# Performance work log

Measured on AMD Instinct MI355X. Metric: run time of the kernel, lower is better.

## Reference

```python
import jax, jax.numpy as jnp
import numpy as np

N = 197          # tokens (== token_count)
B = 64           # batch
D = 768          # d_model
NH = 12          # n_head
GH = 2           # global_heads
HR = NH // GH    # head_ratio = 6
DH = 64          # d_head
QK = GH * DH     # qk_dim = 128
ML = 3           # mask_levels
EPS = 1e-5


def setup_inputs() -> dict:
    key = jax.random.key(0)
    ks = jax.random.split(key, 9)
    s = 1.0 / np.sqrt(D)
    return {
        "h": jax.random.normal(ks[0], (N, B, D), dtype=jnp.float32),
        "masks": jax.random.uniform(ks[1], (N, N, ML), dtype=jnp.float32),
        "Wq": jax.random.normal(ks[2], (QK, D), dtype=jnp.float32) * s,
        "Wk": jax.random.normal(ks[3], (QK, D), dtype=jnp.float32) * s,
        "Wv": jax.random.normal(ks[4], (NH * DH, D), dtype=jnp.float32) * s,
        "Wo": jax.random.normal(ks[5], (D, NH * DH), dtype=jnp.float32) * s,
        "mask_proj": jnp.ones((ML, NH), dtype=jnp.float32),
        "ln_gamma": jnp.ones((D,), dtype=jnp.float32),
        "ln_beta": jnp.zeros((D,), dtype=jnp.float32),
    }


def reference(h, masks, Wq, Wk, Wv, Wo, mask_proj, ln_gamma, ln_beta):
    scale = 1.0 / np.sqrt(DH)
    # projections (seq-first layout [N, B, ...])
    q = (h @ Wq.T).reshape(N, B, GH, DH)
    k = (h @ Wk.T).reshape(N, B, GH, DH)
    v = (h @ Wv.T).reshape(N, B, NH, DH)
    # global-head scores: [B, GH, i, j]
    score = jnp.einsum('ibgd,jbgd->bgij', q, k) * scale
    # learned mask mix: [i, j, NH] -> [GH, i, j, HR] (g-major head split, matches torch reshape)
    mw = jnp.einsum('ijl,ln->ijn', masks, mask_proj)
    mw = mw.reshape(N, N, GH, HR).transpose(2, 0, 1, 3)
    # broadcast each global head to HR local heads: [B, GH, i, j, HR]
    attn = score[..., None] * mw[None]
    attn = attn.transpose(0, 1, 4, 2, 3).reshape(B, NH, N, N)  # head = g*HR + r
    prob = jax.nn.softmax(attn, axis=-1)
    # AV: [i, B, NH, DH] -> [N, B, NH*DH]
    vec = jnp.einsum('bnij,jbnd->ibnd', prob, v).reshape(N, B, NH * DH)
    out = vec @ Wo.T
    # post-LN residual
    x = h + out
    mu = jnp.mean(x, axis=-1, keepdims=True)
    var = jnp.var(x, axis=-1, keepdims=True)
    return ln_gamma * (x - mu) / jnp.sqrt(var + EPS) + ln_beta
```

## Files before the change

### kernel.cpp

```cpp
#include <hip/hip_runtime.h>
#include <hip/hip_bf16.h>
#include <stdint.h>

#define NTOK 197
#define NPAD 224
#define BATCH 64
#define DMODEL 768
#define NHEAD 12
#define GHEAD 2
#define HRATIO 6
#define DHEAD 64
#define QKDIM 128
#define LNEPS 1e-5f
#define MROWS (NTOK * BATCH)
#define MPAD 12672
#define NKC 24
#define NBAND 99

using f32x4 = __attribute__((ext_vector_type(4))) float;
using s16x8 = __attribute__((ext_vector_type(8))) short;
using s16x4 = __attribute__((ext_vector_type(4))) short;

__device__ __forceinline__ short f2bf(float f) {
  unsigned int x = __float_as_uint(f);
  return (short)((x + 0x7fffu + ((x >> 16) & 1u)) >> 16);
}

__device__ __forceinline__ float bf2f(short s) {
  return __uint_as_float((unsigned)(unsigned short)s << 16);
}

__device__ __forceinline__ void gld16(void* lds, const void* g) {
  __builtin_amdgcn_global_load_lds(
      (const __attribute__((address_space(1))) unsigned int*)g,
      (__attribute__((address_space(3))) unsigned int*)lds, 16, 0, 0);
}

#define NBH (NBAND * NKC)
#define NBQ (8 * NKC)
#define NBW (6 * NKC)
__global__ __launch_bounds__(256)
void prep_kernel(const float* __restrict__ h, const float* __restrict__ Wq,
                 const float* __restrict__ Wk, const float* __restrict__ Wv,
                 const float* __restrict__ Wo, short* __restrict__ hf,
                 short* __restrict__ Wqkvf, short* __restrict__ Wof) {
  const int bb = blockIdx.x, t = threadIdx.x;
  int band, kc, which;
  if (bb < NBH) { which = 0; band = bb / NKC; kc = bb - band * NKC; }
  else if (bb < NBH + NBQ) { int i = bb - NBH; which = 1; band = i / NKC; kc = i - band * NKC; }
  else { int i = bb - NBH - NBQ; which = 2; band = i / NKC; kc = i - band * NKC; }
  short* dstS = (which == 0 ? hf : which == 1 ? Wqkvf : Wof) +
                ((size_t)(band * NKC + kc) * 8) * 512;
#pragma unroll
  for (int uu = 0; uu < 2; ++uu) {
    int u = t + uu * 256;
    int frag = u >> 6, l = u & 63;
    int rl = frag * 16 + (l & 15);
    int k0 = kc * 32 + ((l >> 4) & 3) * 8;
    float4 a = {0, 0, 0, 0}, c = {0, 0, 0, 0};
    if (which == 0) {
      int row = band * 128 + rl;
      if (row < MROWS) {
        const float* p = h + (size_t)row * DMODEL + k0;
        a = *(const float4*)p; c = *(const float4*)(p + 4);
      }
    } else if (which == 1) {
      int row = band * 128 + rl;
      const float* src = (row < 128) ? Wq + (size_t)row * DMODEL
                       : (row < 256) ? Wk + (size_t)(row - 128) * DMODEL
                                     : Wv + (size_t)(row - 256) * DMODEL;
      a = *(const float4*)(src + k0); c = *(const float4*)(src + k0 + 4);
    } else {
      const float* p = Wo + (size_t)(band * 128 + rl) * DMODEL + k0;
      a = *(const float4*)p; c = *(const float4*)(p + 4);
    }
    s16x8 o;
    o[0] = f2bf(a.x); o[1] = f2bf(a.y); o[2] = f2bf(a.z); o[3] = f2bf(a.w);
    o[4] = f2bf(c.x); o[5] = f2bf(c.y); o[6] = f2bf(c.z); o[7] = f2bf(c.w);
    *(s16x8*)(dstS + (size_t)u * 8) = o;
  }
}

template<int AM>
__global__ __launch_bounds__(256, 3)
void gemm_bstage_kernel(const short* __restrict__ Af, const short* __restrict__ Bf,
                        short* __restrict__ Cout, int M, int NC) {
  __shared__ short Bs[12 * 4 * 512];
  const int tid = threadIdx.x;
  const int nwg = gridDim.x * gridDim.y;
  const int orig = blockIdx.y * gridDim.x + blockIdx.x;
  const int qq = nwg >> 3, rr = nwg & 7;
  const int xcd = orig & 7, sidx = orig >> 3;
  const int wg = (xcd < rr ? xcd * (qq + 1) : rr * (qq + 1) + (xcd - rr) * qq) + sidx;
  const int cb = wg % gridDim.x;
  const int rb = wg / gridDim.x;

  const int w = tid >> 6, l = tid & 63;
  const int lm = l & 15, lh = l >> 4;

  const short* Bg = Bf + (size_t)(cb >> 1) * NKC * 4096 +
                    ((cb & 1) * 4 + w) * 512 + l * 8;
  const short* paF = Af + (size_t)rb * NKC * 4096 + (2 * w) * 512 + l * 8;
  const short* paR = Af + (size_t)(rb * 128 + w * 32 + lm) * DMODEL + lh * 8;

  f32x4 acc[2][4] = {};

#pragma unroll
  for (int half = 0; half < 2; ++half) {
    if (half) __syncthreads();
#pragma unroll
    for (int p = 0; p < 12; ++p)
      gld16(Bs + (p * 4 + w) * 512 + l * 8, Bg + (size_t)(half * 12 + p) * 4096);
    __syncthreads();
#pragma unroll
    for (int kcl = 0; kcl < 12; ++kcl) {
      const int kc = half * 12 + kcl;
      s16x8 af[2], bf[4];
      if (AM == 0) {
#pragma unroll
        for (int m = 0; m < 2; ++m)
          af[m] = *(const s16x8*)(paF + (size_t)kc * 4096 + m * 512);
      } else {
#pragma unroll
        for (int m = 0; m < 2; ++m)
          af[m] = *(const s16x8*)(paR + (size_t)m * 16 * DMODEL + kc * 32);
      }
#pragma unroll
      for (int n = 0; n < 4; ++n)
        bf[n] = *(const s16x8*)(Bs + (kcl * 4 + n) * 512 + l * 8);
#pragma unroll
      for (int m = 0; m < 2; ++m)
#pragma unroll
        for (int n = 0; n < 4; ++n)
          acc[m][n] = __builtin_amdgcn_mfma_f32_16x16x32_bf16(af[m], bf[n],
                                                              acc[m][n], 0, 0, 0);
    }
  }

#pragma unroll
  for (int m = 0; m < 2; ++m) {
#pragma unroll
    for (int r = 0; r < 4; ++r) {
      int row = rb * 128 + w * 32 + m * 16 + lh * 4 + r;
      if (row < M) {
#pragma unroll
        for (int n = 0; n < 4; ++n) {
          int col = cb * 64 + n * 16 + lm;
          Cout[(size_t)row * NC + col] = f2bf(acc[m][n][r]);
        }
      }
    }
  }
}

__global__ __launch_bounds__(256)
void packall_kernel(const short* __restrict__ Cb, const float* __restrict__ masks,
                    const float* __restrict__ mproj, short* __restrict__ qp,
                    short* __restrict__ kp, short* __restrict__ vT,
                    float* __restrict__ mwp) {
  __shared__ short Vs[NPAD][DHEAD + 1];
  const int bb = blockIdx.x, t = threadIdx.x;
  if (bb < 256) {
    int b = bb >> 2, g = (bb >> 1) & 1, which = bb & 1;
    short* dst = (which ? kp : qp) + ((size_t)b * GHEAD + g) * NPAD * 64;
    int d = t & 63, iofs = t >> 6;
    for (int i0 = 0; i0 < NPAD; i0 += 4) {
      int i = i0 + iofs;
      short v = 0;
      if (i < NTOK)
        v = Cb[(size_t)(i * BATCH + b) * 1024 + which * QKDIM + g * DHEAD + d];
      int dd = which ? ((((d >> 3) ^ (i & 7)) << 3) | (d & 7)) : d;
      dst[i * 64 + dd] = v;
    }
  } else if (bb < 1024) {
    int vv = bb - 256;
    int b = vv / 12, n = vv - b * 12;
    int d = t & 63, iofs = t >> 6;
    for (int i0 = 0; i0 < NPAD; i0 += 4) {
      int i = i0 + iofs;
      short v = 0;
      if (i < NTOK)
        v = Cb[(size_t)(i * BATCH + b) * 1024 + 256 + n * DHEAD + d];
      Vs[i][d] = v;
    }
    __syncthreads();
    short* dst = vT + ((size_t)b * NHEAD + n) * DHEAD * NPAD;
    int sub = t & 63, dr = t >> 6;
    for (int d0 = 0; d0 < DHEAD; d0 += 4) {
      if (sub < 56) {
        int dd = d0 + dr, j0 = sub * 4;
        s16x4 o;
        o[0] = Vs[j0][dd]; o[1] = Vs[j0 + 1][dd];
        o[2] = Vs[j0 + 2][dd]; o[3] = Vs[j0 + 3][dd];
        *(s16x4*)(dst + dd * NPAD + j0) = o;
      }
    }
  } else {
    int e = (bb - 1024) * 256 + t;
    int n = e >> 12;
    int rem = e & 4095;
    int i = rem >> 4, lm = rem & 15;
    float p0 = mproj[n], p1 = mproj[NHEAD + n], p2 = mproj[2 * NHEAD + n];
    float vals[16];
#pragma unroll
    for (int jf = 0; jf < 16; ++jf) vals[jf] = 0.f;
    if (i < NTOK) {
#pragma unroll
      for (int jf = 0; jf < 14; ++jf) {
        int col = jf * 16 + lm;
        if (col < NTOK) {
          const float* mp = masks + ((size_t)i * NTOK + col) * 3;
          vals[jf] = 0.125f * (mp[0] * p0 + mp[1] * p1 + mp[2] * p2);
        }
      }
    }
    float* dst = mwp + (size_t)e * 16;
#pragma unroll
    for (int q = 0; q < 4; ++q) {
      float4 o = make_float4(vals[q * 4], vals[q * 4 + 1], vals[q * 4 + 2], vals[q * 4 + 3]);
      *(float4*)(dst + q * 4) = o;
    }
  }
}

__global__ __launch_bounds__(256, 2)
void attn_fused_kernel(const short* __restrict__ qp, const short* __restrict__ kp,
                       const short* __restrict__ vT, const float* __restrict__ mwp,
                       short* __restrict__ vec_b) {
  const int it = blockIdx.x, b = blockIdx.y, g = blockIdx.z;
  __shared__ short Ks[NPAD * 64];
  __shared__ short Pt[64 * 256];
  __shared__ float rsb[64];
  const int t = threadIdx.x, w = t >> 6, l = t & 63;
  const int lm = l & 15, lh = l >> 4, l7 = l & 7;

  const short* qg = qp + ((size_t)b * GHEAD + g) * NPAD * 64;
  const short* kg = kp + ((size_t)b * GHEAD + g) * NPAD * 64;

#pragma unroll
  for (int s = 0; s < 7; ++s)
    gld16(Ks + s * 2048 + t * 8, kg + s * 2048 + t * 8);
  int qrow = it * 64 + w * 16 + lm;
  if (qrow > NPAD - 1) qrow = NPAD - 1;
  s16x8 a0 = *(const s16x8*)(qg + qrow * 64 + lh * 8);
  s16x8 a1 = *(const s16x8*)(qg + qrow * 64 + 32 + lh * 8);
  __syncthreads();

  f32x4 acc[14] = {};
#pragma unroll
  for (int jf = 0; jf < 14; ++jf) {
    s16x8 kf0 = *(const s16x8*)((const char*)Ks + (jf * 16 + lm) * 128 + ((lh ^ l7) << 4));
    s16x8 kf1 = *(const s16x8*)((const char*)Ks + (jf * 16 + lm) * 128 + (((4 + lh) ^ l7) << 4));
    acc[jf] = __builtin_amdgcn_mfma_f32_16x16x32_bf16(a0, kf0, acc[jf], 0, 0, 0);
    acc[jf] = __builtin_amdgcn_mfma_f32_16x16x32_bf16(a1, kf1, acc[jf], 0, 0, 0);
  }

  for (int hh = 0; hh < HRATIO; ++hh) {
    const int n = g * HRATIO + hh;
    const short* vg = vT + ((size_t)b * NHEAD + n) * 64 * NPAD;
    s16x8 vf[7];
#pragma unroll
    for (int ks = 0; ks < 7; ++ks)
      vf[ks] = *(const s16x8*)(vg + (w * 16 + lm) * NPAD + ks * 32 + lh * 8);

#pragma unroll
    for (int r = 0; r < 4; ++r) {
      const int row = w * 16 + lh * 4 + r;
      const int i = it * 64 + row;
      const float* mr = mwp + (((size_t)n * 256 + i) * 16 + lm) * 16;
      f32x4 mv0 = *(const f32x4*)(mr);
      f32x4 mv1 = *(const f32x4*)(mr + 4);
      f32x4 mv2 = *(const f32x4*)(mr + 8);
      f32x4 mv3 = *(const f32x4*)(mr + 12);
      float sum = 0.f;
#pragma unroll
      for (int jf = 0; jf < 13; ++jf) {
        float mwv = (jf < 4) ? mv0[jf] : (jf < 8) ? mv1[jf - 4]
                  : (jf < 12) ? mv2[jf - 8] : mv3[jf - 12];
        float pe = __expf(acc[jf][r] * mwv);
        if (jf == 12 && lm >= 5) pe = 0.f;
        sum += pe;
        int byteoff = row * 512 + (((2 * jf + (lm >> 3)) ^ (row & 7)) << 4) + (lm & 7) * 2;
        *(short*)((char*)Pt + byteoff) = f2bf(pe);
      }
      {
        int byteoff = row * 512 + (((26 + (lm >> 3)) ^ (row & 7)) << 4) + (lm & 7) * 2;
        *(short*)((char*)Pt + byteoff) = 0;
      }
#pragma unroll
      for (int off = 8; off; off >>= 1) sum += __shfl_xor(sum, off);
      if (lm == 0) rsb[row] = 1.f / sum;
    }
    __syncthreads();

    __builtin_amdgcn_s_setprio(1);
    f32x4 oacc[4] = {};
#pragma unroll
    for (int fi = 0; fi < 4; ++fi)
#pragma unroll
      for (int ks = 0; ks < 7; ++ks) {
        s16x8 pa = *(const s16x8*)((const char*)Pt + (fi * 16 + lm) * 512 +
                                   (((ks * 4 + lh) ^ l7) << 4));
        oacc[fi] = __builtin_amdgcn_mfma_f32_16x16x32_bf16(pa, vf[ks], oacc[fi], 0, 0, 0);
      }
    __builtin_amdgcn_s_setprio(0);
#pragma unroll
    for (int fi = 0; fi < 4; ++fi)
#pragma unroll
      for (int r = 0; r < 4; ++r) {
        int ia = it * 64 + fi * 16 + lh * 4 + r;
        if (ia < NTOK) {
          float rsv = rsb[fi * 16 + lh * 4 + r];
          vec_b[((size_t)ia * BATCH + b) * DMODEL + n * 64 + w * 16 + lm] =
              f2bf(oacc[fi][r] * rsv);
        }
      }
    __syncthreads();
  }
}

__global__ __launch_bounds__(256)
void ln_kernel(const float* __restrict__ h, const short* __restrict__ proj_b,
               float* __restrict__ out, const float* __restrict__ gamma,
               const float* __restrict__ beta) {
  const int m = blockIdx.x;
  const float* hrow = h + (size_t)m * DMODEL;
  const short* prow = proj_b + (size_t)m * DMODEL;
  float* orow = out + (size_t)m * DMODEL;
  const int tid = threadIdx.x;
  float v0 = hrow[tid] + bf2f(prow[tid]);
  float v1 = hrow[tid + 256] + bf2f(prow[tid + 256]);
  float v2 = hrow[tid + 512] + bf2f(prow[tid + 512]);
  float s = v0 + v1 + v2;
  float sq = v0 * v0 + v1 * v1 + v2 * v2;
#pragma unroll
  for (int off = 32; off; off >>= 1) {
    s += __shfl_xor(s, off);
    sq += __shfl_xor(sq, off);
  }
  __shared__ float ss[4], ssq[4];
  const int w = tid >> 6, lane = tid & 63;
  if (lane == 0) { ss[w] = s; ssq[w] = sq; }
  __syncthreads();
  s = ss[0] + ss[1] + ss[2] + ss[3];
  sq = ssq[0] + ssq[1] + ssq[2] + ssq[3];
  const float inv = 1.0f / (float)DMODEL;
  float mu = s * inv;
  float var = sq * inv - mu * mu;
  float rstd = rsqrtf(var + LNEPS);
  orow[tid] = gamma[tid] * (v0 - mu) * rstd + beta[tid];
  orow[tid + 256] = gamma[tid + 256] * (v1 - mu) * rstd + beta[tid + 256];
  orow[tid + 512] = gamma[tid + 512] * (v2 - mu) * rstd + beta[tid + 512];
}

extern "C" void kernel_launch(void* const* d_in, const int* in_sizes, int n_in,
                              void* d_out, int out_size, void* d_ws, size_t ws_size,
                              hipStream_t stream) {
  const float* h     = (const float*)d_in[0];
  const float* masks = (const float*)d_in[1];
  const float* Wq    = (const float*)d_in[2];
  const float* Wk    = (const float*)d_in[3];
  const float* Wv    = (const float*)d_in[4];
  const float* Wo    = (const float*)d_in[5];
  const float* mproj = (const float*)d_in[6];
  const float* gamma = (const float*)d_in[7];
  const float* beta  = (const float*)d_in[8];
  float* out = (float*)d_out;

  char* ws = (char*)d_ws;
  size_t o = 0;
  auto alloc = [&](size_t bytes) { size_t r = o; o += (bytes + 255) & ~(size_t)255; return r; };
  short* hf    = (short*)(ws + alloc((size_t)MPAD * DMODEL * 2));
  short* Cb    = (short*)(ws + alloc((size_t)MPAD * 1024 * 2));
  short* Wqkvf = (short*)(ws + alloc((size_t)1024 * DMODEL * 2));
  short* Wof   = (short*)(ws + alloc((size_t)DMODEL * DMODEL * 2));
  short* qp    = (short*)(ws + alloc((size_t)BATCH * GHEAD * NPAD * DHEAD * 2));
  short* kp    = (short*)(ws + alloc((size_t)BATCH * GHEAD * NPAD * DHEAD * 2));
  short* vT    = (short*)(ws + alloc((size_t)BATCH * NHEAD * DHEAD * NPAD * 2));
  float* mwp   = (float*)(ws + alloc((size_t)NHEAD * 256 * 16 * 16 * 4));
  short* vec_b = hf;
  short* proj_b = Cb;

  prep_kernel<<<NBH + NBQ + NBW, 256, 0, stream>>>(h, Wq, Wk, Wv, Wo, hf, Wqkvf, Wof);
  gemm_bstage_kernel<0><<<dim3(1024 / 64, NBAND), 256, 0, stream>>>(
      hf, Wqkvf, Cb, MROWS, 1024);
  packall_kernel<<<1216, 256, 0, stream>>>(Cb, masks, mproj, qp, kp, vT, mwp);
  attn_fused_kernel<<<dim3(4, BATCH, GHEAD), 256, 0, stream>>>(qp, kp, vT, mwp, vec_b);
  gemm_bstage_kernel<1><<<dim3(DMODEL / 64, NBAND), 256, 0, stream>>>(
      vec_b, Wof, proj_b, MROWS, DMODEL);
  ln_kernel<<<MROWS, 256, 0, stream>>>(h, proj_b, out, gamma, beta);
}
```

Baseline: 152.2 us.

## Replace GEMMs with 256x256-tile double-buffered LDS pipeline using 512 threads

The two projection GEMMs now use 256x256 output tiles with 8 waves per block. A and B k-tiles of width 64 are staged into double-buffered LDS through direct global-to-LDS loads, and the next tile is prefetched while MFMAs run on the current one. The prep kernel is reorganised to emit fragments in the matching 256-row, 64-k tile layout, and setprio is raised around the MFMA bursts. Larger tiles give more reuse per byte loaded. The cost is far fewer blocks (200 and 150), which may underfill the GPU's CUs, plus high register pressure from the 8x4 accumulators.

```diff
diff --git a/kernel.cpp b/kernel.cpp
--- a/kernel.cpp
+++ b/kernel.cpp
@@ -13,9 +13,9 @@
 #define QKDIM 128
 #define LNEPS 1e-5f
 #define MROWS (NTOK * BATCH)
-#define MPAD 12672
-#define NKC 24
-#define NBAND 99
+#define MPAD2 12800
+#define NBAND2 50
+#define NKT 12
 
 using f32x4 = __attribute__((ext_vector_type(4))) float;
 using s16x8 = __attribute__((ext_vector_type(8))) short;
@@ -36,56 +36,56 @@
       (__attribute__((address_space(3))) unsigned int*)lds, 16, 0, 0);
 }
 
-#define NBH (NBAND * NKC)
-#define NBQ (8 * NKC)
-#define NBW (6 * NKC)
+#define NT_A (NBAND2 * NKT)
+#define NT_Q (4 * NKT)
+#define NT_W (3 * NKT)
 __global__ __launch_bounds__(256)
 void prep_kernel(const float* __restrict__ h, const float* __restrict__ Wq,
                  const float* __restrict__ Wk, const float* __restrict__ Wv,
                  const float* __restrict__ Wo, short* __restrict__ hf,
                  short* __restrict__ Wqkvf, short* __restrict__ Wof) {
   const int bb = blockIdx.x, t = threadIdx.x;
-  int band, kc, which;
-  if (bb < NBH) { which = 0; band = bb / NKC; kc = bb - band * NKC; }
-  else if (bb < NBH + NBQ) { int i = bb - NBH; which = 1; band = i / NKC; kc = i - band * NKC; }
-  else { int i = bb - NBH - NBQ; which = 2; band = i / NKC; kc = i - band * NKC; }
-  short* dstS = (which == 0 ? hf : which == 1 ? Wqkvf : Wof) +
-                ((size_t)(band * NKC + kc) * 8) * 512;
-#pragma unroll
-  for (int uu = 0; uu < 2; ++uu) {
-    int u = t + uu * 256;
+  int band, kt, which;
+  if (bb < NT_A) { which = 0; band = bb / NKT; kt = bb - band * NKT; }
+  else if (bb < NT_A + NT_Q) { int i = bb - NT_A; which = 1; band = i / NKT; kt = i - band * NKT; }
+  else { int i = bb - NT_A - NT_Q; which = 2; band = i / NKT; kt = i - band * NKT; }
+  short* dst = (which == 0 ? hf : which == 1 ? Wqkvf : Wof) +
+               (size_t)(band * NKT + kt) * 16384;
+#pragma unroll
+  for (int ff = 0; ff < 8; ++ff) {
+    int u = ff * 256 + t;
     int frag = u >> 6, l = u & 63;
-    int rl = frag * 16 + (l & 15);
-    int k0 = kc * 32 + ((l >> 4) & 3) * 8;
+    int mf = frag & 15;
+    int kf = frag >> 4;
+    int row = band * 256 + mf * 16 + (l & 15);
+    int k0 = kt * 64 + kf * 32 + ((l >> 4) & 3) * 8;
     float4 a = {0, 0, 0, 0}, c = {0, 0, 0, 0};
     if (which == 0) {
-      int row = band * 128 + rl;
       if (row < MROWS) {
         const float* p = h + (size_t)row * DMODEL + k0;
         a = *(const float4*)p; c = *(const float4*)(p + 4);
       }
     } else if (which == 1) {
-      int row = band * 128 + rl;
       const float* src = (row < 128) ? Wq + (size_t)row * DMODEL
                        : (row < 256) ? Wk + (size_t)(row - 128) * DMODEL
                                      : Wv + (size_t)(row - 256) * DMODEL;
       a = *(const float4*)(src + k0); c = *(const float4*)(src + k0 + 4);
     } else {
-      const float* p = Wo + (size_t)(band * 128 + rl) * DMODEL + k0;
+      const float* p = Wo + (size_t)row * DMODEL + k0;
       a = *(const float4*)p; c = *(const float4*)(p + 4);
     }
     s16x8 o;
     o[0] = f2bf(a.x); o[1] = f2bf(a.y); o[2] = f2bf(a.z); o[3] = f2bf(a.w);
     o[4] = f2bf(c.x); o[5] = f2bf(c.y); o[6] = f2bf(c.z); o[7] = f2bf(c.w);
-    *(s16x8*)(dstS + (size_t)u * 8) = o;
+    *(s16x8*)(dst + (size_t)u * 8) = o;
   }
 }
 
 template<int AM>
-__global__ __launch_bounds__(256, 3)
-void gemm_bstage_kernel(const short* __restrict__ Af, const short* __restrict__ Bf,
-                        short* __restrict__ Cout, int M, int NC) {
-  __shared__ short Bs[12 * 4 * 512];
+__global__ __launch_bounds__(512)
+void gemm256_kernel(const short* __restrict__ Af, const short* __restrict__ Bf,
+                    short* __restrict__ Cout, int M, int NC) {
+  __shared__ short Ls[2][2][16384];
   const int tid = threadIdx.x;
   const int nwg = gridDim.x * gridDim.y;
   const int orig = blockIdx.y * gridDim.x + blockIdx.x;
@@ -96,56 +96,69 @@
   const int rb = wg / gridDim.x;
 
   const int w = tid >> 6, l = tid & 63;
+  const int wr = w >> 2, wc = w & 3;
   const int lm = l & 15, lh = l >> 4;
 
-  const short* Bg = Bf + (size_t)(cb >> 1) * NKC * 4096 +
-                    ((cb & 1) * 4 + w) * 512 + l * 8;
-  const short* paF = Af + (size_t)rb * NKC * 4096 + (2 * w) * 512 + l * 8;
-  const short* paR = Af + (size_t)(rb * 128 + w * 32 + lm) * DMODEL + lh * 8;
-
-  f32x4 acc[2][4] = {};
-
-#pragma unroll
-  for (int half = 0; half < 2; ++half) {
-    if (half) __syncthreads();
-#pragma unroll
-    for (int p = 0; p < 12; ++p)
-      gld16(Bs + (p * 4 + w) * 512 + l * 8, Bg + (size_t)(half * 12 + p) * 4096);
-    __syncthreads();
-#pragma unroll
-    for (int kcl = 0; kcl < 12; ++kcl) {
-      const int kc = half * 12 + kcl;
-      s16x8 af[2], bf[4];
-      if (AM == 0) {
-#pragma unroll
-        for (int m = 0; m < 2; ++m)
-          af[m] = *(const s16x8*)(paF + (size_t)kc * 4096 + m * 512);
-      } else {
-#pragma unroll
-        for (int m = 0; m < 2; ++m)
-          af[m] = *(const s16x8*)(paR + (size_t)m * 16 * DMODEL + kc * 32);
-      }
+  const short* Ag = Af + (size_t)rb * (NKT * 16384);
+  const short* Bg = Bf + (size_t)cb * (NKT * 16384);
+  const short* paR = Af + (size_t)(rb * 256 + wr * 128 + lm) * DMODEL + lh * 8;
+
+  f32x4 acc[8][4] = {};
+
+#define STG(buf, kt)                                                          \
+  do {                                                                        \
+    if (AM == 0) {                                                            \
+      _Pragma("unroll") for (int s = 0; s < 4; ++s)                           \
+        gld16(&Ls[buf][0][s * 4096 + tid * 8],                                \
+              Ag + (size_t)(kt) * 16384 + s * 4096 + tid * 8);                \
+    }                                                                         \
+    _Pragma("unroll") for (int s = 0; s < 4; ++s)                             \
+      gld16(&Ls[buf][1][s * 4096 + tid * 8],                                  \
+            Bg + (size_t)(kt) * 16384 + s * 4096 + tid * 8);                  \
+  } while (0)
+
+  STG(0, 0);
+  asm volatile("s_waitcnt vmcnt(0)" ::: "memory");
+  __builtin_amdgcn_s_barrier();
+
+  for (int kt = 0; kt < NKT; ++kt) {
+    const int cur = kt & 1;
+    if (kt + 1 < NKT) STG(cur ^ 1, kt + 1);
+#pragma unroll
+    for (int kf = 0; kf < 2; ++kf) {
+      s16x8 bfr[4];
 #pragma unroll
       for (int n = 0; n < 4; ++n)
-        bf[n] = *(const s16x8*)(Bs + (kcl * 4 + n) * 512 + l * 8);
-#pragma unroll
-      for (int m = 0; m < 2; ++m)
+        bfr[n] = *(const s16x8*)&Ls[cur][1][((kf * 16 + wc * 4 + n) * 64 + l) * 8];
+      __builtin_amdgcn_s_setprio(1);
+#pragma unroll
+      for (int m = 0; m < 8; ++m) {
+        s16x8 afr;
+        if (AM == 0)
+          afr = *(const s16x8*)&Ls[cur][0][((kf * 16 + wr * 8 + m) * 64 + l) * 8];
+        else
+          afr = *(const s16x8*)(paR + (size_t)m * 16 * DMODEL + kt * 64 + kf * 32);
 #pragma unroll
         for (int n = 0; n < 4; ++n)
-          acc[m][n] = __builtin_amdgcn_mfma_f32_16x16x32_bf16(af[m], bf[n],
+          acc[m][n] = __builtin_amdgcn_mfma_f32_16x16x32_bf16(afr, bfr[n],
                                                               acc[m][n], 0, 0, 0);
-    }
-  }
-
-#pragma unroll
-  for (int m = 0; m < 2; ++m) {
+      }
+      __builtin_amdgcn_s_setprio(0);
+    }
+    asm volatile("s_waitcnt vmcnt(0) lgkmcnt(0)" ::: "memory");
+    __builtin_amdgcn_s_barrier();
+  }
+#undef STG
+
+#pragma unroll
+  for (int m = 0; m < 8; ++m) {
 #pragma unroll
     for (int r = 0; r < 4; ++r) {
-      int row = rb * 128 + w * 32 + m * 16 + lh * 4 + r;
+      int row = rb * 256 + wr * 128 + m * 16 + lh * 4 + r;
       if (row < M) {
 #pragma unroll
         for (int n = 0; n < 4; ++n) {
-          int col = cb * 64 + n * 16 + lm;
+          int col = cb * 256 + wc * 64 + n * 16 + lm;
           Cout[(size_t)row * NC + col] = f2bf(acc[m][n][r]);
         }
       }
@@ -370,8 +383,8 @@
   char* ws = (char*)d_ws;
   size_t o = 0;
   auto alloc = [&](size_t bytes) { size_t r = o; o += (bytes + 255) & ~(size_t)255; return r; };
-  short* hf    = (short*)(ws + alloc((size_t)MPAD * DMODEL * 2));
-  short* Cb    = (short*)(ws + alloc((size_t)MPAD * 1024 * 2));
+  short* hf    = (short*)(ws + alloc((size_t)MPAD2 * DMODEL * 2));
+  short* Cb    = (short*)(ws + alloc((size_t)MROWS * 1024 * 2));
   short* Wqkvf = (short*)(ws + alloc((size_t)1024 * DMODEL * 2));
   short* Wof   = (short*)(ws + alloc((size_t)DMODEL * DMODEL * 2));
   short* qp    = (short*)(ws + alloc((size_t)BATCH * GHEAD * NPAD * DHEAD * 2));
@@ -381,12 +394,10 @@
   short* vec_b = hf;
   short* proj_b = Cb;
 
-  prep_kernel<<<NBH + NBQ + NBW, 256, 0, stream>>>(h, Wq, Wk, Wv, Wo, hf, Wqkvf, Wof);
-  gemm_bstage_kernel<0><<<dim3(1024 / 64, NBAND), 256, 0, stream>>>(
-      hf, Wqkvf, Cb, MROWS, 1024);
+  prep_kernel<<<NT_A + NT_Q + NT_W, 256, 0, stream>>>(h, Wq, Wk, Wv, Wo, hf, Wqkvf, Wof);
+  gemm256_kernel<0><<<dim3(4, NBAND2), 512, 0, stream>>>(hf, Wqkvf, Cb, MROWS, 1024);
   packall_kernel<<<1216, 256, 0, stream>>>(Cb, masks, mproj, qp, kp, vT, mwp);
   attn_fused_kernel<<<dim3(4, BATCH, GHEAD), 256, 0, stream>>>(qp, kp, vT, mwp, vec_b);
-  gemm_bstage_kernel<1><<<dim3(DMODEL / 64, NBAND), 256, 0, stream>>>(
-      vec_b, Wof, proj_b, MROWS, DMODEL);
+  gemm256_kernel<1><<<dim3(3, NBAND2), 512, 0, stream>>>(vec_b, Wof, proj_b, MROWS, DMODEL);
   ln_kernel<<<MROWS, 256, 0, stream>>>(h, proj_b, out, gamma, beta);
 }
```

Result: slower. 169.6 us (+11.5%).
